# Kernel optimization log

Measured on AMD Instinct MI355X. Metric: run time of the kernel, lower is better.

The kernel has to match this reference:

```python
import jax, jax.numpy as jnp
import numpy as np

B, T, H, NH, E = 4, 1024, 1024, 16, 8
DH = H // NH
S = B * T
CAP = int(np.ceil(S * 1.0 / E))  # capacity_factor=1.0, k=1


def _ln(x, w, b, eps=1e-5):
    m = x.mean(-1, keepdims=True)
    v = x.var(-1, keepdims=True)
    return (x - m) * jax.lax.rsqrt(v + eps) * w + b


def _attn(h, in_w, in_b, out_w, out_b):
    qkv = h @ in_w.T + in_b                               # [B,T,3H]
    q, k, v = jnp.split(qkv, 3, axis=-1)
    hd = lambda t: t.reshape(B, T, NH, DH).transpose(0, 2, 1, 3)  # [B,NH,T,DH]
    q, k, v = hd(q), hd(k), hd(v)
    scores = jnp.einsum('bhqd,bhkd->bhqk', q, k) / np.float32(np.sqrt(DH))
    p = jax.nn.softmax(scores, axis=-1)
    o = jnp.einsum('bhqk,bhkd->bhqd', p, v)
    o = o.transpose(0, 2, 1, 3).reshape(B, T, H)
    return o @ out_w.T + out_b


def _moe(h, wg, w1, b1, w2, b2):
    xt = h.reshape(S, H)
    gates = jax.nn.softmax(xt @ wg, axis=-1)              # [S,E]
    eidx = jnp.argmax(gates, axis=-1)                     # [S] chosen expert
    mask1 = jax.nn.one_hot(eidx, E, dtype=jnp.int32)      # [S,E]
    locs = jnp.cumsum(mask1, axis=0) - 1                  # slot within expert
    pos = jnp.sum(locs * mask1, axis=-1)                  # [S]
    keep = pos < CAP                                      # capacity drop
    gval = jnp.take_along_axis(gates, eidx[:, None], axis=-1)[:, 0] * keep
    posc = jnp.minimum(pos, CAP - 1)
    contrib = jnp.where(keep[:, None], xt, jnp.zeros((), xt.dtype))
    disp = jnp.zeros((E, CAP, H), xt.dtype).at[eidx, posc].add(contrib)  # [E,C,H]
    hmid = jax.nn.gelu(jnp.einsum('ech,ehf->ecf', disp, w1) + b1[:, None, :], approximate=False)
    eout = jnp.einsum('ecf,efh->ech', hmid, w2) + b2[:, None, :]          # [E,C,H]
    y = eout[eidx, posc] * gval[:, None]                  # dropped tokens -> gval=0
    return y.reshape(B, T, H)


def setup_inputs() -> dict:
    key = jax.random.key(0)
    ks = jax.random.split(key, 6)
    s = 0.02
    return {
        'x': jax.random.normal(ks[0], (B, T, H), jnp.float32),
        'ln1_w': jnp.ones((H,), jnp.float32),
        'ln1_b': jnp.zeros((H,), jnp.float32),
        'in_proj_w': jax.random.normal(ks[1], (3 * H, H), jnp.float32) * s,
        'in_proj_b': jnp.zeros((3 * H,), jnp.float32),
        'out_proj_w': jax.random.normal(ks[2], (H, H), jnp.float32) * s,
        'out_proj_b': jnp.zeros((H,), jnp.float32),
        'ln2_w': jnp.ones((H,), jnp.float32),
        'ln2_b': jnp.zeros((H,), jnp.float32),
        'wg': jax.random.normal(ks[3], (H, E), jnp.float32) * s,
        'w1': jax.random.normal(ks[4], (E, H, 4 * H), jnp.float32) * s,
        'b1': jnp.zeros((E, 4 * H), jnp.float32),
        'w2': jax.random.normal(ks[5], (E, 4 * H, H), jnp.float32) * s,
        'b2': jnp.zeros((E, H), jnp.float32),
    }


def reference(x, ln1_w, ln1_b, in_proj_w, in_proj_b, out_proj_w, out_proj_b,
              ln2_w, ln2_b, wg, w1, b1, w2, b2):
    h = _ln(x, ln1_w, ln1_b)
    x = x + _attn(h, in_proj_w, in_proj_b, out_proj_w, out_proj_b)
    h = _ln(x, ln2_w, ln2_b)
    return x + _moe(h, wg, w1, b1, w2, b2)
```

## Files before the change

kernel.cpp:

```cpp
#include <hip/hip_runtime.h>
#include <hip/hip_bf16.h>


#define Bc   4
#define Tc   1024
#define Hc   1024
#define NHc  16
#define DHc  64
#define Ec   8
#define CAPc 512
#define Sc   4096
#define FFc  4096

typedef __attribute__((ext_vector_type(8))) short bf16x8;
typedef __attribute__((ext_vector_type(4))) float f32x4;

#define LDP 40

__device__ __forceinline__ float gelu_exact(float x) {
    return 0.5f * x * (1.0f + erff(x * 0.70710678118654752440f));
}

__device__ __forceinline__ ushort f2bf(float f) {
    union { __hip_bfloat16 h; ushort u; } c;
    c.h = __float2bfloat16(f);
    return c.u;
}

__device__ __forceinline__ ushort4 pack4(float a, float b, float c, float d) {
    ushort4 r;
    r.x = f2bf(a); r.y = f2bf(b); r.z = f2bf(c); r.w = f2bf(d);
    return r;
}

template <int OUTBF>
__global__ __launch_bounds__(256) void ln_kernel(const float* __restrict__ x,
                                                 const float* __restrict__ w,
                                                 const float* __restrict__ b,
                                                 void* __restrict__ o) {
    const int row = blockIdx.x;
    const int tid = threadIdx.x;
    const float4 v = ((const float4*)(x + (size_t)row * Hc))[tid];
    float s = v.x + v.y + v.z + v.w;
    float q = v.x * v.x + v.y * v.y + v.z * v.z + v.w * v.w;
#pragma unroll
    for (int m = 1; m < 64; m <<= 1) {
        s += __shfl_xor(s, m);
        q += __shfl_xor(q, m);
    }
    __shared__ float ss[4], qq[4];
    if ((tid & 63) == 0) { ss[tid >> 6] = s; qq[tid >> 6] = q; }
    __syncthreads();
    s = ss[0] + ss[1] + ss[2] + ss[3];
    q = qq[0] + qq[1] + qq[2] + qq[3];
    const float mean = s * (1.0f / Hc);
    const float var  = q * (1.0f / Hc) - mean * mean;
    const float inv  = 1.0f / sqrtf(var + 1e-5f);
    const float4 wv = ((const float4*)w)[tid];
    const float4 bv = ((const float4*)b)[tid];
    float4 r;
    r.x = (v.x - mean) * inv * wv.x + bv.x;
    r.y = (v.y - mean) * inv * wv.y + bv.y;
    r.z = (v.z - mean) * inv * wv.z + bv.z;
    r.w = (v.w - mean) * inv * wv.w + bv.w;
    if (OUTBF) {
        ((ushort4*)((ushort*)o + (size_t)row * Hc))[tid] = pack4(r.x, r.y, r.z, r.w);
    } else {
        ((float4*)((float*)o + (size_t)row * Hc))[tid] = r;
    }
}

template <int BLAYOUT, int EPI, int OUTBF>
__global__ __launch_bounds__(256) void mgemm(const ushort* __restrict__ Ag,
                                             const float* __restrict__ Bg,
                                             const float* __restrict__ biasg,
                                             const float* __restrict__ resg,
                                             void* __restrict__ Cg,
                                             int M, int N, int K,
                                             long long sA, long long sB,
                                             long long sC, long long sBias) {
    const int e = blockIdx.z;
    const ushort* A    = Ag + (size_t)e * sA;
    const float*  B    = Bg + (size_t)e * sB;
    const float*  bias = biasg + (size_t)e * sBias;

    const int m0 = blockIdx.y * 128;
    const int n0 = blockIdx.x * 128;
    const int tid  = threadIdx.x;
    const int lane = tid & 63;
    const int wid  = tid >> 6;
    const int wm   = wid >> 1;
    const int wn   = wid & 1;
    const int lg   = lane >> 4;
    const int lr   = lane & 15;

    __shared__ ushort As[128 * LDP];
    __shared__ ushort Bs[128 * LDP];

    f32x4 acc[4][4];
#pragma unroll
    for (int i = 0; i < 4; ++i)
#pragma unroll
        for (int j = 0; j < 4; ++j) acc[i][j] = (f32x4){0.f, 0.f, 0.f, 0.f};

    const int asub = tid & 3;
    const int bn  = tid >> 1;
    const int bkh = (tid & 1) * 16;

    for (int k0 = 0; k0 < K; k0 += 32) {
        __syncthreads();
#pragma unroll
        for (int j = 0; j < 2; ++j) {
            const int row = (tid >> 2) + j * 64;
            const uint4 v = *(const uint4*)(A + (size_t)(m0 + row) * K + k0 + asub * 8);
            *(uint4*)&As[row * LDP + asub * 8] = v;
        }
        if (BLAYOUT == 0) {
#pragma unroll
            for (int q = 0; q < 4; ++q) {
                const float4 v = *(const float4*)(B + (size_t)(n0 + bn) * K + k0 + bkh + q * 4);
                *(ushort4*)&Bs[bn * LDP + bkh + q * 4] = pack4(v.x, v.y, v.z, v.w);
            }
        } else {
            float vv[16];
#pragma unroll
            for (int kk = 0; kk < 16; ++kk)
                vv[kk] = B[(size_t)(k0 + bkh + kk) * N + n0 + bn];
#pragma unroll
            for (int q = 0; q < 4; ++q)
                *(ushort4*)&Bs[bn * LDP + bkh + q * 4] =
                    pack4(vv[q * 4], vv[q * 4 + 1], vv[q * 4 + 2], vv[q * 4 + 3]);
        }
        __syncthreads();

        bf16x8 af[4], bfr[4];
#pragma unroll
        for (int t = 0; t < 4; ++t) {
            af[t]  = *(const bf16x8*)&As[(wm * 64 + t * 16 + lr) * LDP + lg * 8];
            bfr[t] = *(const bf16x8*)&Bs[(wn * 64 + t * 16 + lr) * LDP + lg * 8];
        }
#pragma unroll
        for (int mt = 0; mt < 4; ++mt)
#pragma unroll
            for (int nt = 0; nt < 4; ++nt)
                acc[mt][nt] = __builtin_amdgcn_mfma_f32_16x16x32_bf16(
                    af[mt], bfr[nt], acc[mt][nt], 0, 0, 0);
    }

#pragma unroll
    for (int nt = 0; nt < 4; ++nt) {
        const int n = n0 + wn * 64 + nt * 16 + lr;
        const float bv = bias[n];
#pragma unroll
        for (int mt = 0; mt < 4; ++mt) {
#pragma unroll
            for (int r = 0; r < 4; ++r) {
                const int m = m0 + wm * 64 + mt * 16 + lg * 4 + r;
                float v = acc[mt][nt][r] + bv;
                if constexpr (EPI == 1) v = gelu_exact(v);
                if constexpr (EPI == 2) v += resg[(size_t)m * N + n];
                if constexpr (OUTBF) {
                    ((ushort*)Cg)[(size_t)e * sC + (size_t)m * N + n] = f2bf(v);
                } else {
                    ((float*)Cg)[(size_t)e * sC + (size_t)m * N + n] = v;
                }
            }
        }
    }
}

__global__ __launch_bounds__(256) void attn_kernel(const float* __restrict__ qkv,
                                                   ushort* __restrict__ o) {
    const int qt = blockIdx.x;
    const int bh = blockIdx.y;
    const int bb = bh >> 4;
    const int hh = bh & 15;
    const int tid = threadIdx.x;
    const int r0 = (tid >> 4) * 4;
    const int c0 = (tid & 15) * 4;

    __shared__ float Qt[64][68];
    __shared__ float Kt[64][68];
    __shared__ float Vs[64][68];
    __shared__ float Ps[64][65];

    const size_t base = (size_t)bb * Tc * 3072 + hh * 64;

#pragma unroll
    for (int jj = 0; jj < 4; ++jj) {
        const int idx = tid + jj * 256;
        const int rr = idx >> 4;
        const int cc = (idx & 15) * 4;
        const float4 v = *(const float4*)(qkv + base + (size_t)(qt * 64 + rr) * 3072 + cc);
        Qt[cc + 0][rr] = v.x;
        Qt[cc + 1][rr] = v.y;
        Qt[cc + 2][rr] = v.z;
        Qt[cc + 3][rr] = v.w;
    }

    float m[4], l[4], acc[4][4];
#pragma unroll
    for (int i = 0; i < 4; ++i) {
        m[i] = -1e30f;
        l[i] = 0.0f;
#pragma unroll
        for (int j = 0; j < 4; ++j) acc[i][j] = 0.0f;
    }

    for (int kt = 0; kt < 16; ++kt) {
        __syncthreads();
#pragma unroll
        for (int jj = 0; jj < 4; ++jj) {
            const int idx = tid + jj * 256;
            const int rr = idx >> 4;
            const int cc = (idx & 15) * 4;
            const float* kp = qkv + base + (size_t)(kt * 64 + rr) * 3072 + Hc + cc;
            const float4 kv = *(const float4*)kp;
            const float4 vv = *(const float4*)(kp + Hc);
            Kt[cc + 0][rr] = kv.x;
            Kt[cc + 1][rr] = kv.y;
            Kt[cc + 2][rr] = kv.z;
            Kt[cc + 3][rr] = kv.w;
            *(float4*)&Vs[rr][cc] = vv;
        }
        __syncthreads();

        float sv[4][4];
#pragma unroll
        for (int i = 0; i < 4; ++i)
#pragma unroll
            for (int j = 0; j < 4; ++j) sv[i][j] = 0.0f;

#pragma unroll 8
        for (int d = 0; d < 64; ++d) {
            const float4 qv = *(const float4*)&Qt[d][r0];
            const float4 kv = *(const float4*)&Kt[d][c0];
            const float qa[4] = {qv.x, qv.y, qv.z, qv.w};
            const float ka[4] = {kv.x, kv.y, kv.z, kv.w};
#pragma unroll
            for (int i = 0; i < 4; ++i)
#pragma unroll
                for (int j = 0; j < 4; ++j) sv[i][j] = fmaf(qa[i], ka[j], sv[i][j]);
        }

#pragma unroll
        for (int i = 0; i < 4; ++i) {
#pragma unroll
            for (int j = 0; j < 4; ++j) sv[i][j] *= 0.125f;
            float mx = fmaxf(fmaxf(sv[i][0], sv[i][1]), fmaxf(sv[i][2], sv[i][3]));
#pragma unroll
            for (int msk = 1; msk < 16; msk <<= 1) mx = fmaxf(mx, __shfl_xor(mx, msk));
            const float mn = fmaxf(m[i], mx);
            const float sc = expf(m[i] - mn);
            float rs = 0.0f;
#pragma unroll
            for (int j = 0; j < 4; ++j) {
                const float p = expf(sv[i][j] - mn);
                sv[i][j] = p;
                rs += p;
            }
#pragma unroll
            for (int msk = 1; msk < 16; msk <<= 1) rs += __shfl_xor(rs, msk);
            l[i] = l[i] * sc + rs;
            m[i] = mn;
#pragma unroll
            for (int j = 0; j < 4; ++j) acc[i][j] *= sc;
            Ps[r0 + i][c0 + 0] = sv[i][0];
            Ps[r0 + i][c0 + 1] = sv[i][1];
            Ps[r0 + i][c0 + 2] = sv[i][2];
            Ps[r0 + i][c0 + 3] = sv[i][3];
        }
        __syncthreads();

#pragma unroll 4
        for (int k = 0; k < 64; ++k) {
            const float p0 = Ps[r0 + 0][k];
            const float p1 = Ps[r0 + 1][k];
            const float p2 = Ps[r0 + 2][k];
            const float p3 = Ps[r0 + 3][k];
            const float4 vv = *(const float4*)&Vs[k][c0];
            acc[0][0] = fmaf(p0, vv.x, acc[0][0]);
            acc[0][1] = fmaf(p0, vv.y, acc[0][1]);
            acc[0][2] = fmaf(p0, vv.z, acc[0][2]);
            acc[0][3] = fmaf(p0, vv.w, acc[0][3]);
            acc[1][0] = fmaf(p1, vv.x, acc[1][0]);
            acc[1][1] = fmaf(p1, vv.y, acc[1][1]);
            acc[1][2] = fmaf(p1, vv.z, acc[1][2]);
            acc[1][3] = fmaf(p1, vv.w, acc[1][3]);
            acc[2][0] = fmaf(p2, vv.x, acc[2][0]);
            acc[2][1] = fmaf(p2, vv.y, acc[2][1]);
            acc[2][2] = fmaf(p2, vv.z, acc[2][2]);
            acc[2][3] = fmaf(p2, vv.w, acc[2][3]);
            acc[3][0] = fmaf(p3, vv.x, acc[3][0]);
            acc[3][1] = fmaf(p3, vv.y, acc[3][1]);
            acc[3][2] = fmaf(p3, vv.z, acc[3][2]);
            acc[3][3] = fmaf(p3, vv.w, acc[3][3]);
        }
    }

#pragma unroll
    for (int i = 0; i < 4; ++i) {
        const float inv = 1.0f / l[i];
        *(ushort4*)(o + (size_t)(bb * Tc + qt * 64 + r0 + i) * Hc + hh * 64 + c0) =
            pack4(acc[i][0] * inv, acc[i][1] * inv, acc[i][2] * inv, acc[i][3] * inv);
    }
}

__global__ __launch_bounds__(256) void gate_kernel(const float* __restrict__ h2,
                                                   const float* __restrict__ wg,
                                                   int* __restrict__ eidx,
                                                   float* __restrict__ gvr) {
    const int s = blockIdx.x;
    const int tid = threadIdx.x;
    const float4 hv = ((const float4*)(h2 + (size_t)s * Hc))[tid];
    const float hx[4] = {hv.x, hv.y, hv.z, hv.w};
    float p[8];
#pragma unroll
    for (int e2 = 0; e2 < 8; ++e2) p[e2] = 0.0f;
#pragma unroll
    for (int i = 0; i < 4; ++i) {
        const int k = tid * 4 + i;
        const float4 w0 = *(const float4*)(wg + (size_t)k * 8);
        const float4 w1 = *(const float4*)(wg + (size_t)k * 8 + 4);
        p[0] = fmaf(hx[i], w0.x, p[0]);
        p[1] = fmaf(hx[i], w0.y, p[1]);
        p[2] = fmaf(hx[i], w0.z, p[2]);
        p[3] = fmaf(hx[i], w0.w, p[3]);
        p[4] = fmaf(hx[i], w1.x, p[4]);
        p[5] = fmaf(hx[i], w1.y, p[5]);
        p[6] = fmaf(hx[i], w1.z, p[6]);
        p[7] = fmaf(hx[i], w1.w, p[7]);
    }
#pragma unroll
    for (int e2 = 0; e2 < 8; ++e2)
#pragma unroll
        for (int msk = 1; msk < 64; msk <<= 1) p[e2] += __shfl_xor(p[e2], msk);
    __shared__ float lg[4][8];
    if ((tid & 63) == 0) {
#pragma unroll
        for (int e2 = 0; e2 < 8; ++e2) lg[tid >> 6][e2] = p[e2];
    }
    __syncthreads();
    if (tid == 0) {
        float l[8];
#pragma unroll
        for (int e2 = 0; e2 < 8; ++e2) l[e2] = lg[0][e2] + lg[1][e2] + lg[2][e2] + lg[3][e2];
        int best = 0;
        float bm = l[0];
#pragma unroll
        for (int e2 = 1; e2 < 8; ++e2)
            if (l[e2] > bm) { bm = l[e2]; best = e2; }
        float se = 0.0f;
#pragma unroll
        for (int e2 = 0; e2 < 8; ++e2) se += expf(l[e2] - bm);
        eidx[s] = best;
        gvr[s] = 1.0f / se;
    }
}

__global__ __launch_bounds__(256) void route_kernel(const int* __restrict__ eidx,
                                                    const float* __restrict__ gvr,
                                                    int* __restrict__ posc,
                                                    float* __restrict__ gval,
                                                    int* __restrict__ s2t,
                                                    int* __restrict__ counts) {
    __shared__ int running[8];
    __shared__ unsigned long long wb[8][4];
    const int tid = threadIdx.x;
    const int wave = tid >> 6;
    const int lane = tid & 63;
    if (tid < 8) running[tid] = 0;
    __syncthreads();
    for (int chunk = 0; chunk < Sc / 256; ++chunk) {
        const int s = chunk * 256 + tid;
        const int e = eidx[s];
#pragma unroll
        for (int ex = 0; ex < 8; ++ex) {
            const unsigned long long bl = __ballot(e == ex);
            if (lane == 0) wb[ex][wave] = bl;
        }
        __syncthreads();
        int before = running[e];
#pragma unroll
        for (int w = 0; w < 4; ++w) {
            const unsigned long long bw = wb[e][w];
            if (w < wave) before += __popcll(bw);
            else if (w == wave) before += __popcll(bw & ((1ull << lane) - 1ull));
        }
        const int pos = before;
        const int keep = pos < CAPc;
        posc[s] = keep ? pos : (CAPc - 1);
        gval[s] = keep ? gvr[s] : 0.0f;
        if (keep) s2t[e * CAPc + pos] = s;
        __syncthreads();
        if (tid < 8) {
            int tot = 0;
#pragma unroll
            for (int w = 0; w < 4; ++w) tot += __popcll(wb[tid][w]);
            running[tid] += tot;
        }
        __syncthreads();
    }
    if (tid < 8) counts[tid] = running[tid];
}

__global__ __launch_bounds__(256) void dispatch_kernel(const float* __restrict__ h2,
                                                       const int* __restrict__ s2t,
                                                       const int* __restrict__ counts,
                                                       ushort* __restrict__ disp) {
    const int slot = blockIdx.x;
    const int e = slot >> 9;
    const int c = slot & (CAPc - 1);
    int cnt = counts[e];
    cnt = cnt > CAPc ? CAPc : cnt;
    ushort4* dst = (ushort4*)(disp + (size_t)slot * Hc);
    if (c < cnt) {
        const int s = s2t[slot];
        const float4 v = ((const float4*)(h2 + (size_t)s * Hc))[threadIdx.x];
        dst[threadIdx.x] = pack4(v.x, v.y, v.z, v.w);
    } else {
        dst[threadIdx.x] = make_ushort4(0, 0, 0, 0);
    }
}

__global__ __launch_bounds__(256) void gather_kernel(const float* __restrict__ x1,
                                                     const float* __restrict__ eout,
                                                     const int* __restrict__ eidx,
                                                     const int* __restrict__ posc,
                                                     const float* __restrict__ gval,
                                                     float* __restrict__ out) {
    const int s = blockIdx.x;
    const float g = gval[s];
    const int slot = eidx[s] * CAPc + posc[s];
    const float4 a = ((const float4*)(x1 + (size_t)s * Hc))[threadIdx.x];
    const float4 b = ((const float4*)(eout + (size_t)slot * Hc))[threadIdx.x];
    float4 r;
    r.x = a.x + b.x * g;
    r.y = a.y + b.y * g;
    r.z = a.z + b.z * g;
    r.w = a.w + b.w * g;
    ((float4*)(out + (size_t)s * Hc))[threadIdx.x] = r;
}

extern "C" void kernel_launch(void* const* d_in, const int* in_sizes, int n_in,
                              void* d_out, int out_size, void* d_ws, size_t ws_size,
                              hipStream_t stream) {
    const float* x     = (const float*)d_in[0];
    const float* ln1_w = (const float*)d_in[1];
    const float* ln1_b = (const float*)d_in[2];
    const float* in_w  = (const float*)d_in[3];
    const float* in_b  = (const float*)d_in[4];
    const float* out_w = (const float*)d_in[5];
    const float* out_b = (const float*)d_in[6];
    const float* ln2_w = (const float*)d_in[7];
    const float* ln2_b = (const float*)d_in[8];
    const float* wg    = (const float*)d_in[9];
    const float* w1    = (const float*)d_in[10];
    const float* b1    = (const float*)d_in[11];
    const float* w2    = (const float*)d_in[12];
    const float* b2    = (const float*)d_in[13];
    float* out = (float*)d_out;
    float* ws  = (float*)d_ws;

    const size_t SH = (size_t)Sc * Hc;
    float*  qkv_f  = ws;
    ushort* hmid_u = (ushort*)ws;
    float*  r1     = ws + 3 * SH;
    ushort* hA     = (ushort*)r1;
    float*  r2     = r1 + SH / 2;
    float*  h2     = r2;
    float*  eout   = r2;
    float*  smallf = r2 + SH;
    float* gvr  = smallf;
    float* gval = gvr + Sc;
    int* eidx   = (int*)(gval + Sc);
    int* posc   = eidx + Sc;
    int* s2t    = posc + Sc;
    int* counts = s2t + Ec * CAPc;

    float* x1 = out;

    ln_kernel<1><<<Sc, 256, 0, stream>>>(x, ln1_w, ln1_b, hA);
    mgemm<0, 0, 0><<<dim3(24, 32, 1), 256, 0, stream>>>(
        hA, in_w, in_b, nullptr, qkv_f, Sc, 3 * Hc, Hc, 0, 0, 0, 0);
    attn_kernel<<<dim3(Tc / 64, Bc * NHc), 256, 0, stream>>>(qkv_f, hA);
    mgemm<0, 2, 0><<<dim3(8, 32, 1), 256, 0, stream>>>(
        hA, out_w, out_b, x, x1, Sc, Hc, Hc, 0, 0, 0, 0);
    ln_kernel<0><<<Sc, 256, 0, stream>>>(x1, ln2_w, ln2_b, h2);
    gate_kernel<<<Sc, 256, 0, stream>>>(h2, wg, eidx, gvr);
    route_kernel<<<1, 256, 0, stream>>>(eidx, gvr, posc, gval, s2t, counts);
    dispatch_kernel<<<Ec * CAPc, 256, 0, stream>>>(h2, s2t, counts, hA);
    mgemm<1, 1, 1><<<dim3(32, 4, Ec), 256, 0, stream>>>(
        hA, w1, b1, nullptr, hmid_u, CAPc, FFc, Hc,
        (long long)CAPc * Hc, (long long)Hc * FFc, (long long)CAPc * FFc, FFc);
    mgemm<1, 0, 0><<<dim3(8, 4, Ec), 256, 0, stream>>>(
        hmid_u, w2, b2, nullptr, eout, CAPc, Hc, FFc,
        (long long)CAPc * FFc, (long long)FFc * Hc, (long long)CAPc * Hc, Hc);
    gather_kernel<<<Sc, 256, 0, stream>>>(x1, eout, eidx, posc, gval, out);
}
```

Measured before the change: 1.037 ms.

## Rewrite attention with bf16 MFMA and emit QKV projection in bf16

Replaces the scalar fp32 flash-attention kernel with one that computes QK^T and PV using 16x16x32 bf16 MFMA instructions. K tiles are staged row-major and V is transposed into shared memory. The QKV projection GEMM now writes bf16 instead of fp32, which halves the intermediate traffic and feeds the MFMA path directly. This trades precision in the attention probabilities and Q/K/V for matrix-core throughput, and the transposed V stores into shared memory may cause bank conflicts.

```diff
diff --git a/kernel.cpp b/kernel.cpp
--- a/kernel.cpp
+++ b/kernel.cpp
@@ -169,140 +169,111 @@
     }
 }
 
-__global__ __launch_bounds__(256) void attn_kernel(const float* __restrict__ qkv,
-                                                   ushort* __restrict__ o) {
+__global__ __launch_bounds__(256) void mattn(const ushort* __restrict__ qkv,
+                                             ushort* __restrict__ o) {
     const int qt = blockIdx.x;
     const int bh = blockIdx.y;
     const int bb = bh >> 4;
     const int hh = bh & 15;
-    const int tid = threadIdx.x;
-    const int r0 = (tid >> 4) * 4;
-    const int c0 = (tid & 15) * 4;
-
-    __shared__ float Qt[64][68];
-    __shared__ float Kt[64][68];
-    __shared__ float Vs[64][68];
-    __shared__ float Ps[64][65];
-
-    const size_t base = (size_t)bb * Tc * 3072 + hh * 64;
-
-#pragma unroll
-    for (int jj = 0; jj < 4; ++jj) {
-        const int idx = tid + jj * 256;
-        const int rr = idx >> 4;
-        const int cc = (idx & 15) * 4;
-        const float4 v = *(const float4*)(qkv + base + (size_t)(qt * 64 + rr) * 3072 + cc);
-        Qt[cc + 0][rr] = v.x;
-        Qt[cc + 1][rr] = v.y;
-        Qt[cc + 2][rr] = v.z;
-        Qt[cc + 3][rr] = v.w;
-    }
-
-    float m[4], l[4], acc[4][4];
-#pragma unroll
-    for (int i = 0; i < 4; ++i) {
-        m[i] = -1e30f;
-        l[i] = 0.0f;
-#pragma unroll
-        for (int j = 0; j < 4; ++j) acc[i][j] = 0.0f;
-    }
+    const int tid  = threadIdx.x;
+    const int lane = tid & 63;
+    const int w    = tid >> 6;
+    const int lg   = lane >> 4;
+    const int lr   = lane & 15;
+
+    __shared__ ushort Ks[64 * 72];
+    __shared__ ushort Vt[64 * 72];
+    __shared__ ushort Ps[64 * 72];
+
+    const size_t base = (size_t)bb * Tc * 3072 + (size_t)hh * 64;
+
+    bf16x8 qf[2];
+    {
+        const ushort* qrow = qkv + base + (size_t)(qt * 64 + w * 16 + lr) * 3072;
+        qf[0] = *(const bf16x8*)(qrow + lg * 8);
+        qf[1] = *(const bf16x8*)(qrow + 32 + lg * 8);
+    }
+
+    float mreg[4], lreg[4];
+    f32x4 oacc[4];
+#pragma unroll
+    for (int r = 0; r < 4; ++r) { mreg[r] = -1e30f; lreg[r] = 0.0f; }
+#pragma unroll
+    for (int d = 0; d < 4; ++d) oacc[d] = (f32x4){0.f, 0.f, 0.f, 0.f};
 
     for (int kt = 0; kt < 16; ++kt) {
         __syncthreads();
 #pragma unroll
-        for (int jj = 0; jj < 4; ++jj) {
-            const int idx = tid + jj * 256;
-            const int rr = idx >> 4;
-            const int cc = (idx & 15) * 4;
-            const float* kp = qkv + base + (size_t)(kt * 64 + rr) * 3072 + Hc + cc;
-            const float4 kv = *(const float4*)kp;
-            const float4 vv = *(const float4*)(kp + Hc);
-            Kt[cc + 0][rr] = kv.x;
-            Kt[cc + 1][rr] = kv.y;
-            Kt[cc + 2][rr] = kv.z;
-            Kt[cc + 3][rr] = kv.w;
-            *(float4*)&Vs[rr][cc] = vv;
-        }
-        __syncthreads();
-
-        float sv[4][4];
-#pragma unroll
-        for (int i = 0; i < 4; ++i)
-#pragma unroll
-            for (int j = 0; j < 4; ++j) sv[i][j] = 0.0f;
-
-#pragma unroll 8
-        for (int d = 0; d < 64; ++d) {
-            const float4 qv = *(const float4*)&Qt[d][r0];
-            const float4 kv = *(const float4*)&Kt[d][c0];
-            const float qa[4] = {qv.x, qv.y, qv.z, qv.w};
-            const float ka[4] = {kv.x, kv.y, kv.z, kv.w};
-#pragma unroll
-            for (int i = 0; i < 4; ++i)
-#pragma unroll
-                for (int j = 0; j < 4; ++j) sv[i][j] = fmaf(qa[i], ka[j], sv[i][j]);
-        }
-
-#pragma unroll
-        for (int i = 0; i < 4; ++i) {
-#pragma unroll
-            for (int j = 0; j < 4; ++j) sv[i][j] *= 0.125f;
-            float mx = fmaxf(fmaxf(sv[i][0], sv[i][1]), fmaxf(sv[i][2], sv[i][3]));
+        for (int j = 0; j < 2; ++j) {
+            const int c   = tid + j * 256;
+            const int key = c >> 3;
+            const int dc  = c & 7;
+            const ushort* krow = qkv + base + (size_t)(kt * 64 + key) * 3072;
+            const uint4 kv = *(const uint4*)(krow + Hc + dc * 8);
+            const uint4 vv = *(const uint4*)(krow + 2 * Hc + dc * 8);
+            *(uint4*)&Ks[key * 72 + dc * 8] = kv;
+            union { uint4 v; ushort u[8]; } cv;
+            cv.v = vv;
+#pragma unroll
+            for (int jj = 0; jj < 8; ++jj) Vt[(dc * 8 + jj) * 72 + key] = cv.u[jj];
+        }
+        __syncthreads();
+
+        f32x4 s[4];
+#pragma unroll
+        for (int f = 0; f < 4; ++f) s[f] = (f32x4){0.f, 0.f, 0.f, 0.f};
+#pragma unroll
+        for (int ks = 0; ks < 2; ++ks) {
+#pragma unroll
+            for (int f = 0; f < 4; ++f) {
+                const bf16x8 kf = *(const bf16x8*)&Ks[(f * 16 + lr) * 72 + ks * 32 + lg * 8];
+                s[f] = __builtin_amdgcn_mfma_f32_16x16x32_bf16(qf[ks], kf, s[f], 0, 0, 0);
+            }
+        }
+
+#pragma unroll
+        for (int r = 0; r < 4; ++r) {
+            float s0 = s[0][r] * 0.125f, s1 = s[1][r] * 0.125f;
+            float s2 = s[2][r] * 0.125f, s3 = s[3][r] * 0.125f;
+            float mx = fmaxf(fmaxf(s0, s1), fmaxf(s2, s3));
 #pragma unroll
             for (int msk = 1; msk < 16; msk <<= 1) mx = fmaxf(mx, __shfl_xor(mx, msk));
-            const float mn = fmaxf(m[i], mx);
-            const float sc = expf(m[i] - mn);
-            float rs = 0.0f;
-#pragma unroll
-            for (int j = 0; j < 4; ++j) {
-                const float p = expf(sv[i][j] - mn);
-                sv[i][j] = p;
-                rs += p;
+            const float mn = fmaxf(mreg[r], mx);
+            const float sc = expf(mreg[r] - mn);
+            const float p0 = expf(s0 - mn), p1 = expf(s1 - mn);
+            const float p2 = expf(s2 - mn), p3 = expf(s3 - mn);
+            float rs = p0 + p1 + p2 + p3;
+#pragma unroll
+            for (int msk = 1; msk < 16; msk <<= 1) rs += __shfl_xor(rs, msk);
+            lreg[r] = lreg[r] * sc + rs;
+            mreg[r] = mn;
+#pragma unroll
+            for (int d = 0; d < 4; ++d) oacc[d][r] *= sc;
+            const int prow = (w * 16 + lg * 4 + r) * 72;
+            Ps[prow + 0 * 16 + lr] = f2bf(p0);
+            Ps[prow + 1 * 16 + lr] = f2bf(p1);
+            Ps[prow + 2 * 16 + lr] = f2bf(p2);
+            Ps[prow + 3 * 16 + lr] = f2bf(p3);
+        }
+
+#pragma unroll
+        for (int ks = 0; ks < 2; ++ks) {
+            const bf16x8 pa = *(const bf16x8*)&Ps[(w * 16 + lr) * 72 + ks * 32 + lg * 8];
+#pragma unroll
+            for (int d = 0; d < 4; ++d) {
+                const bf16x8 vf = *(const bf16x8*)&Vt[(d * 16 + lr) * 72 + ks * 32 + lg * 8];
+                oacc[d] = __builtin_amdgcn_mfma_f32_16x16x32_bf16(pa, vf, oacc[d], 0, 0, 0);
             }
-#pragma unroll
-            for (int msk = 1; msk < 16; msk <<= 1) rs += __shfl_xor(rs, msk);
-            l[i] = l[i] * sc + rs;
-            m[i] = mn;
-#pragma unroll
-            for (int j = 0; j < 4; ++j) acc[i][j] *= sc;
-            Ps[r0 + i][c0 + 0] = sv[i][0];
-            Ps[r0 + i][c0 + 1] = sv[i][1];
-            Ps[r0 + i][c0 + 2] = sv[i][2];
-            Ps[r0 + i][c0 + 3] = sv[i][3];
-        }
-        __syncthreads();
-
-#pragma unroll 4
-        for (int k = 0; k < 64; ++k) {
-            const float p0 = Ps[r0 + 0][k];
-            const float p1 = Ps[r0 + 1][k];
-            const float p2 = Ps[r0 + 2][k];
-            const float p3 = Ps[r0 + 3][k];
-            const float4 vv = *(const float4*)&Vs[k][c0];
-            acc[0][0] = fmaf(p0, vv.x, acc[0][0]);
-            acc[0][1] = fmaf(p0, vv.y, acc[0][1]);
-            acc[0][2] = fmaf(p0, vv.z, acc[0][2]);
-            acc[0][3] = fmaf(p0, vv.w, acc[0][3]);
-            acc[1][0] = fmaf(p1, vv.x, acc[1][0]);
-            acc[1][1] = fmaf(p1, vv.y, acc[1][1]);
-            acc[1][2] = fmaf(p1, vv.z, acc[1][2]);
-            acc[1][3] = fmaf(p1, vv.w, acc[1][3]);
-            acc[2][0] = fmaf(p2, vv.x, acc[2][0]);
-            acc[2][1] = fmaf(p2, vv.y, acc[2][1]);
-            acc[2][2] = fmaf(p2, vv.z, acc[2][2]);
-            acc[2][3] = fmaf(p2, vv.w, acc[2][3]);
-            acc[3][0] = fmaf(p3, vv.x, acc[3][0]);
-            acc[3][1] = fmaf(p3, vv.y, acc[3][1]);
-            acc[3][2] = fmaf(p3, vv.z, acc[3][2]);
-            acc[3][3] = fmaf(p3, vv.w, acc[3][3]);
-        }
-    }
-
-#pragma unroll
-    for (int i = 0; i < 4; ++i) {
-        const float inv = 1.0f / l[i];
-        *(ushort4*)(o + (size_t)(bb * Tc + qt * 64 + r0 + i) * Hc + hh * 64 + c0) =
-            pack4(acc[i][0] * inv, acc[i][1] * inv, acc[i][2] * inv, acc[i][3] * inv);
+        }
+    }
+
+#pragma unroll
+    for (int r = 0; r < 4; ++r) {
+        const float inv = 1.0f / lreg[r];
+        const size_t grow = (size_t)(bb * Tc + qt * 64 + w * 16 + lg * 4 + r) * Hc + hh * 64;
+#pragma unroll
+        for (int d = 0; d < 4; ++d)
+            o[grow + d * 16 + lr] = f2bf(oacc[d][r] * inv);
     }
 }
 
@@ -463,7 +434,7 @@
     float* ws  = (float*)d_ws;
 
     const size_t SH = (size_t)Sc * Hc;
-    float*  qkv_f  = ws;
+    ushort* qkv_u  = (ushort*)ws;
     ushort* hmid_u = (ushort*)ws;
     float*  r1     = ws + 3 * SH;
     ushort* hA     = (ushort*)r1;
@@ -481,9 +452,9 @@
     float* x1 = out;
 
     ln_kernel<1><<<Sc, 256, 0, stream>>>(x, ln1_w, ln1_b, hA);
-    mgemm<0, 0, 0><<<dim3(24, 32, 1), 256, 0, stream>>>(
-        hA, in_w, in_b, nullptr, qkv_f, Sc, 3 * Hc, Hc, 0, 0, 0, 0);
-    attn_kernel<<<dim3(Tc / 64, Bc * NHc), 256, 0, stream>>>(qkv_f, hA);
+    mgemm<0, 0, 1><<<dim3(24, 32, 1), 256, 0, stream>>>(
+        hA, in_w, in_b, nullptr, qkv_u, Sc, 3 * Hc, Hc, 0, 0, 0, 0);
+    mattn<<<dim3(Tc / 64, Bc * NHc), 256, 0, stream>>>(qkv_u, hA);
     mgemm<0, 2, 0><<<dim3(8, 32, 1), 256, 0, stream>>>(
         hA, out_w, out_b, x, x1, Sc, Hc, Hc, 0, 0, 0, 0);
     ln_kernel<0><<<Sc, 256, 0, stream>>>(x1, ln2_w, ln2_b, h2);
```

Result: faster. 839.5 us (-19.0%).
